# Kernel tuning notes

Measured on AMD Instinct MI355X. Metric: run time of the kernel, lower is better.

The kernel has to match this reference:

```python
import jax, jax.numpy as jnp
import numpy as np

B_SZ = 2
D_MODEL = 1024
H = 16
C = 8
BLK = 128
DK = 64
DV = 64
NCHUNK = 1024            # tokens per chunk (divisible by BLK)
T = C * (1 + NCHUNK)     # 8200: [g0, chunk0..., g1, chunk1..., ...]


def setup_inputs() -> dict:
    key = jax.random.key(0)
    k0, k1, k2, k3, k4 = jax.random.split(key, 5)
    s = 0.02
    x  = jax.random.normal(k0, (B_SZ, T, D_MODEL), dtype=jnp.float32)
    Wq = jax.random.normal(k1, (D_MODEL, H * DK), dtype=jnp.float32) * s
    Wk = jax.random.normal(k2, (D_MODEL, H * DK), dtype=jnp.float32) * s
    Wv = jax.random.normal(k3, (D_MODEL, H * DV), dtype=jnp.float32) * s
    Wo = jax.random.normal(k4, (H * DV, D_MODEL), dtype=jnp.float32) * s
    bo = jnp.zeros((D_MODEL,), dtype=jnp.float32)
    return {"x": x, "Wq": Wq, "Wk": Wk, "Wv": Wv, "Wo": Wo, "bo": bo}


def _local_sparse_3block(qf, kf, vf):
    # qf,kf: [BC, H, N, dk], vf: [BC, H, N, dv]; window = [left, current, right] blocks
    bc, h, n, dk = qf.shape
    dv = vf.shape[-1]
    nb = n // BLK
    q = qf.reshape(bc, h, nb, BLK, dk)
    k = kf.reshape(bc, h, nb, BLK, dk)
    v = vf.reshape(bc, h, nb, BLK, dv)
    zk = jnp.zeros((bc, h, 1, BLK, dk), qf.dtype)
    zv = jnp.zeros((bc, h, 1, BLK, dv), qf.dtype)
    kp = jnp.concatenate([zk, k, zk], axis=2)          # [bc,h,nb+2,B,dk]
    vp = jnp.concatenate([zv, v, zv], axis=2)
    k_win = jnp.concatenate([kp[:, :, 0:nb], kp[:, :, 1:nb + 1], kp[:, :, 2:nb + 2]], axis=3)  # [bc,h,nb,3B,dk]
    v_win = jnp.concatenate([vp[:, :, 0:nb], vp[:, :, 1:nb + 1], vp[:, :, 2:nb + 2]], axis=3)  # [bc,h,nb,3B,dv]
    scale = 1.0 / np.sqrt(dk).astype(np.float32)
    scores = jnp.einsum('bhnqd,bhnkd->bhnqk', q, k_win) * scale   # [bc,h,nb,B,3B]
    mask = np.zeros((nb, 3 * BLK), dtype=bool)
    mask[0, :BLK] = True           # first block: left padding invalid
    mask[-1, 2 * BLK:] = True      # last block: right padding invalid
    scores = jnp.where(jnp.asarray(mask)[None, None, :, None, :], -jnp.inf, scores)
    attn = jax.nn.softmax(scores, axis=-1)
    out = jnp.einsum('bhnqk,bhnkd->bhnqd', attn, v_win)
    return out.reshape(bc, h, n, dv)


def reference(x, Wq, Wk, Wv, Wo, bo):
    Bb, Tt, _ = x.shape
    q = (x @ Wq).reshape(Bb, Tt, H, DK).transpose(0, 2, 1, 3)  # [B,H,T,dk]
    k = (x @ Wk).reshape(Bb, Tt, H, DK).transpose(0, 2, 1, 3)
    v = (x @ Wv).reshape(Bb, Tt, H, DV).transpose(0, 2, 1, 3)
    stride = NCHUNK + 1
    g_idx = jnp.arange(C) * stride
    gq = q[:, :, g_idx]  # [B,H,C,dk]
    gk = k[:, :, g_idx]
    gv = v[:, :, g_idx]  # [B,H,C,dv]
    local_idx = ((g_idx + 1)[:, None] + jnp.arange(NCHUNK)[None, :]).reshape(-1)
    qx = q[:, :, local_idx].reshape(Bb, H, C, NCHUNK, DK)
    kx = k[:, :, local_idx].reshape(Bb, H, C, NCHUNK, DK)
    vx = v[:, :, local_idx].reshape(Bb, H, C, NCHUNK, DV)
    # local 3-block attention per chunk
    q_flat = qx.transpose(0, 2, 1, 3, 4).reshape(Bb * C, H, NCHUNK, DK)
    k_flat = kx.transpose(0, 2, 1, 3, 4).reshape(Bb * C, H, NCHUNK, DK)
    v_flat = vx.transpose(0, 2, 1, 3, 4).reshape(Bb * C, H, NCHUNK, DV)
    out_local = _local_sparse_3block(q_flat, k_flat, v_flat)
    out_local = out_local.reshape(Bb, C, H, NCHUNK, DV).transpose(0, 2, 1, 3, 4)  # [B,H,C,Nchunk,dv]
    # each local token additionally receives its chunk's global value directly
    out_chunks = out_local + gv[:, :, :, None, :]
    # global tokens attend over all globals + own chunk's locals (joint softmax, fp32)
    scale = 1.0 / np.sqrt(DK).astype(np.float32)
    scores_gg = jnp.einsum('bhcd,bhed->bhce', gq, gk) * scale      # [B,H,C,C]
    scores_gl = jnp.einsum('bhcd,bhcnd->bhcn', gq, kx) * scale     # [B,H,C,Nchunk]
    attn = jax.nn.softmax(jnp.concatenate([scores_gg, scores_gl], axis=-1), axis=-1)
    a_gg, a_gl = attn[..., :C], attn[..., C:]
    out_g = (jnp.einsum('bhce,bhed->bhcd', a_gg, gv)
             + jnp.einsum('bhcn,bhcnd->bhcd', a_gl, vx))           # [B,H,C,dv]
    out_inter = jnp.concatenate([out_g[:, :, :, None, :], out_chunks], axis=3)  # [B,H,C,1+Nchunk,dv]
    out = out_inter.reshape(Bb, H, Tt, DV).transpose(0, 2, 1, 3).reshape(Bb, Tt, H * DV)
    return out @ Wo + bo
```

## Files before the change

kernel.cpp:

```cpp
#include <hip/hip_runtime.h>
#include <hip/hip_bf16.h>

typedef __bf16 bf16x8 __attribute__((ext_vector_type(8)));
typedef float  f32x4  __attribute__((ext_vector_type(4)));
typedef unsigned short u16x8 __attribute__((ext_vector_type(8)));
typedef unsigned short u16x4 __attribute__((ext_vector_type(4)));
typedef unsigned u32x4 __attribute__((ext_vector_type(4)));
typedef unsigned long long u64x2 __attribute__((ext_vector_type(2)));

#define T_TOK   8200
#define M_TOK   16400
#define QKV_LD  3072
#define DM      1024

#define AS1CU const __attribute__((address_space(1))) unsigned int*
#define AS3U  __attribute__((address_space(3))) unsigned int*
#define GLDS16(g, s) __builtin_amdgcn_global_load_lds((AS1CU)(g), (AS3U)(s), 16, 0, 0)

__device__ __forceinline__ unsigned short f2bf(float f){
  __hip_bfloat16 h = __float2bfloat16(f);
  return *reinterpret_cast<unsigned short*>(&h);
}
__device__ __forceinline__ float bf2f(unsigned short u){
  union { unsigned u; float f; } x; x.u = ((unsigned)u) << 16;
  return x.f;
}

__global__ __launch_bounds__(256) void k_prep(const float* __restrict__ x, unsigned short* __restrict__ xb,
                                              const float* __restrict__ Wq, const float* __restrict__ Wk,
                                              const float* __restrict__ Wv, const float* __restrict__ Wo,
                                              unsigned short* __restrict__ wqkvt, unsigned short* __restrict__ wot){
  __shared__ float t[64][65];
  int bid = blockIdx.x, tid = threadIdx.x;
  if (bid < 2048){
    const long n4 = (long)M_TOK * 1024 / 4;
    long i = (long)bid * 256 + tid;
    const long stride = 2048L * 256;
    for (long e = i; e < n4; e += stride){
      float4 v = ((const float4*)x)[e];
      u16x4 o; o[0]=f2bf(v.x); o[1]=f2bf(v.y); o[2]=f2bf(v.z); o[3]=f2bf(v.w);
      ((u16x4*)xb)[e] = o;
    }
    return;
  }
  int bid2 = bid - 2048;
  int z = bid2 & 3; int rest = bid2 >> 2;
  int bx = rest & 15, by = rest >> 4;
  const float* W; unsigned short* Wt;
  if      (z == 0){ W = Wq; Wt = wqkvt; }
  else if (z == 1){ W = Wk; Wt = wqkvt + (size_t)1024*1024; }
  else if (z == 2){ W = Wv; Wt = wqkvt + (size_t)2048*1024; }
  else            { W = Wo; Wt = wot; }
  int tk0 = bx * 64, tn0 = by * 64;
#pragma unroll
  for (int i = 0; i < 4; i++){
    int ch = tid + i*256; int kr = ch >> 4, n4i = (ch & 15) * 4;
    float4 v = *(const float4*)(W + (size_t)(tk0+kr)*1024 + tn0 + n4i);
    t[kr][n4i+0]=v.x; t[kr][n4i+1]=v.y; t[kr][n4i+2]=v.z; t[kr][n4i+3]=v.w;
  }
  __syncthreads();
#pragma unroll
  for (int i = 0; i < 4; i++){
    int ch = tid + i*256; int nr = ch >> 4, k4 = (ch & 15) * 4;
    u16x4 o;
#pragma unroll
    for (int e = 0; e < 4; e++) o[e] = f2bf(t[k4+e][nr]);
    *(u16x4*)(Wt + (size_t)(tn0+nr)*1024 + tk0 + k4) = o;
  }
}

__global__ __launch_bounds__(256,2) void k_gemm(const unsigned short* __restrict__ A,
                                                const unsigned short* __restrict__ Bt,
                                                const float* __restrict__ bias,
                                                void* __restrict__ Cout,
                                                int M, int K, int ldc, int bf16out, int gn){
  __shared__ unsigned short As[128][64];
  __shared__ unsigned short Bs[128][64];
  int tid = threadIdx.x, l = tid & 63, w = tid >> 6;
  int li = l & 15, lh = l >> 4;
  int nwg = gridDim.x;
  int wg = (blockIdx.x & 7) * (nwg >> 3) + (blockIdx.x >> 3);
  int m0 = (wg / gn) * 128, n0 = (wg % gn) * 128;
  int wm = (w & 1) * 64, wn = (w >> 1) * 64;
  int lr = l >> 3, lc = l & 7;
  int lsw = li & 7;

  f32x4 acc[4][4];
#pragma unroll
  for (int a = 0; a < 4; a++)
#pragma unroll
    for (int b = 0; b < 4; b++) acc[a][b] = 0.f;

  for (int kt = 0; kt < K; kt += 64){
    __syncthreads();
#pragma unroll
    for (int i = 0; i < 4; i++){
      int r = w*32 + i*8 + lr;
      int colsw = (lc ^ (r & 7)) * 8;
      int rga = m0 + r; if (rga >= M) rga = M - 1;
      GLDS16(A  + (size_t)rga     *K + kt + colsw, &As[w*32 + i*8][0]);
      GLDS16(Bt + (size_t)(n0 + r)*K + kt + colsw, &Bs[w*32 + i*8][0]);
    }
    __syncthreads();
#pragma unroll
    for (int ks = 0; ks < 2; ks++){
      bf16x8 af[4], bfr[4];
#pragma unroll
      for (int mt = 0; mt < 4; mt++)
        af[mt] = *(const bf16x8*)&As[wm + mt*16 + li][((ks*4 + lh) ^ lsw) * 8];
#pragma unroll
      for (int nt = 0; nt < 4; nt++)
        bfr[nt] = *(const bf16x8*)&Bs[wn + nt*16 + li][((ks*4 + lh) ^ lsw) * 8];
#pragma unroll
      for (int mt = 0; mt < 4; mt++)
#pragma unroll
        for (int nt = 0; nt < 4; nt++)
          acc[mt][nt] = __builtin_amdgcn_mfma_f32_16x16x32_bf16(af[mt], bfr[nt], acc[mt][nt], 0, 0, 0);
    }
  }
#pragma unroll
  for (int mt = 0; mt < 4; mt++)
#pragma unroll
    for (int nt = 0; nt < 4; nt++)
#pragma unroll
      for (int r = 0; r < 4; r++){
        int row = m0 + wm + mt*16 + lh*4 + r;
        int col = n0 + wn + nt*16 + li;
        if (row < M){
          float v = acc[mt][nt][r] + (bias ? bias[col] : 0.f);
          if (bf16out) ((unsigned short*)Cout)[(size_t)row*ldc + col] = f2bf(v);
          else         ((float*)Cout)[(size_t)row*ldc + col] = v;
        }
      }
}

__global__ __launch_bounds__(256,3) void k_local(const unsigned short* __restrict__ qkv,
                                                 unsigned short* __restrict__ att){
  __shared__ unsigned short Ks[128][64];
  __shared__ unsigned short Vt[64][136];

  int tid = threadIdx.x;

  if (blockIdx.x < 256){
    float* sc   = (float*)&Ks[0][0];
    float* red  = sc + 1032;
    float* gq_s = red + 256;
    int gid = blockIdx.x;
    int c = gid & 7, h = (gid >> 3) & 15, b = gid >> 7;
    size_t bT = (size_t)b * T_TOK;
    size_t grow = bT + (size_t)c*1025;
    if (tid < 64) gq_s[tid] = bf2f(qkv[grow*QKV_LD + h*64 + tid]);
    __syncthreads();
    float lmax = -3e38f;
    for (int idx = tid; idx < 1032; idx += 256){
      size_t krow = (idx < 8) ? (bT + (size_t)idx*1025) : (bT + (size_t)c*1025 + 1 + (idx - 8));
      const unsigned short* kp = qkv + krow*QKV_LD + 1024 + h*64;
      float s = 0.f;
#pragma unroll
      for (int d0 = 0; d0 < 64; d0 += 8){
        u16x8 kv = *(const u16x8*)(kp + d0);
#pragma unroll
        for (int e = 0; e < 8; e++) s += gq_s[d0+e] * bf2f(kv[e]);
      }
      s *= 0.125f;
      sc[idx] = s;
      lmax = fmaxf(lmax, s);
    }
    red[tid] = lmax; __syncthreads();
    for (int st = 128; st > 0; st >>= 1){ if (tid < st) red[tid] = fmaxf(red[tid], red[tid+st]); __syncthreads(); }
    float m = red[0]; __syncthreads();
    float lsum = 0.f;
    for (int idx = tid; idx < 1032; idx += 256){
      float p = __expf(sc[idx] - m); sc[idx] = p; lsum += p;
    }
    red[tid] = lsum; __syncthreads();
    for (int st = 128; st > 0; st >>= 1){ if (tid < st) red[tid] += red[tid+st]; __syncthreads(); }
    float denom = red[0]; __syncthreads();
    int d = tid & 63, part = tid >> 6;
    float acc = 0.f;
    for (int idx = part; idx < 1032; idx += 4){
      size_t krow = (idx < 8) ? (bT + (size_t)idx*1025) : (bT + (size_t)c*1025 + 1 + (idx - 8));
      acc += sc[idx] * bf2f(qkv[krow*QKV_LD + 2048 + h*64 + d]);
    }
    red[tid] = acc; __syncthreads();
    if (tid < 64){
      float o = (red[tid] + red[tid+64] + red[tid+128] + red[tid+192]) / denom;
      att[grow*DM + h*64 + tid] = f2bf(o);
    }
    return;
  }

  int l = tid & 63, w = tid >> 6;
  int li = l & 15, lh = l >> 4;
  int lr = l >> 3, lc = l & 7;
  int lsw = li & 7;
  int wg0 = blockIdx.x - 256;
  int wg = (wg0 & 7) * 256 + (wg0 >> 3);
  int blk = wg & 7, c = (wg >> 3) & 7, h = (wg >> 6) & 15, b = wg >> 10;
  size_t bT = (size_t)b * T_TOK;
  int tokq0 = c*1025 + 1 + blk*128;

  bf16x8 aq[2][2];
#pragma unroll
  for (int tr = 0; tr < 2; tr++)
#pragma unroll
    for (int ks = 0; ks < 2; ks++)
      aq[tr][ks] = *(const bf16x8*)(qkv + (bT + tokq0 + w*32 + tr*16 + li)*QKV_LD + h*64 + ks*32 + lh*8);

  float psum[2] = {0.f, 0.f};
  f32x4 oacc[2][4];
#pragma unroll
  for (int tr = 0; tr < 2; tr++)
#pragma unroll
    for (int ct = 0; ct < 4; ct++) oacc[tr][ct] = 0.f;

  for (int kb = blk-1; kb <= blk+1; ++kb){
    if ((unsigned)kb > 7u) continue;
    int tokk0 = c*1025 + 1 + kb*128;

    u16x8 vlo[2], vhi[2];
#pragma unroll
    for (int i = 0; i < 2; i++){
      int gv = 4*i + w;
      const unsigned short* vp = qkv + (bT + tokk0 + 2*l)*QKV_LD + 2048 + h*64 + gv*8;
      vlo[i] = *(const u16x8*)vp;
      vhi[i] = *(const u16x8*)(vp + QKV_LD);
    }
    __syncthreads();
#pragma unroll
    for (int i = 0; i < 4; i++){
      int r = w*32 + i*8 + lr;
      int colk = (lc ^ (r & 7)) * 8;
      GLDS16(qkv + (bT + tokk0 + r)*QKV_LD + 1024 + h*64 + colk, &Ks[w*32 + i*8][0]);
    }
#pragma unroll
    for (int i = 0; i < 2; i++)
#pragma unroll
      for (int e = 0; e < 8; e++){
        unsigned pk = (unsigned)vlo[i][e] | ((unsigned)vhi[i][e] << 16);
        *(unsigned*)&Vt[(4*i + w)*8 + e][2*l] = pk;
      }
    __syncthreads();

    f32x4 s2[2][8];
#pragma unroll
    for (int tr = 0; tr < 2; tr++)
#pragma unroll
      for (int ct = 0; ct < 8; ct++) s2[tr][ct] = 0.f;
#pragma unroll
    for (int ct = 0; ct < 8; ct++)
#pragma unroll
      for (int ks = 0; ks < 2; ks++){
        bf16x8 kf = *(const bf16x8*)&Ks[ct*16 + li][((ks*4 + lh) ^ lsw) * 8];
        s2[0][ct] = __builtin_amdgcn_mfma_f32_16x16x32_bf16(kf, aq[0][ks], s2[0][ct], 0, 0, 0);
        s2[1][ct] = __builtin_amdgcn_mfma_f32_16x16x32_bf16(kf, aq[1][ks], s2[1][ct], 0, 0, 0);
      }

#pragma unroll
    for (int ks = 0; ks < 4; ks++){
      bf16x8 pa[2];
#pragma unroll
      for (int tr = 0; tr < 2; tr++){
        float q0 = __expf(s2[tr][2*ks  ][0] * 0.125f);
        float q1 = __expf(s2[tr][2*ks  ][1] * 0.125f);
        float q2 = __expf(s2[tr][2*ks  ][2] * 0.125f);
        float q3 = __expf(s2[tr][2*ks  ][3] * 0.125f);
        float q4 = __expf(s2[tr][2*ks+1][0] * 0.125f);
        float q5 = __expf(s2[tr][2*ks+1][1] * 0.125f);
        float q6 = __expf(s2[tr][2*ks+1][2] * 0.125f);
        float q7 = __expf(s2[tr][2*ks+1][3] * 0.125f);
        psum[tr] += ((q0 + q1) + (q2 + q3)) + ((q4 + q5) + (q6 + q7));
        u32x4 frv;
        frv.x = (unsigned)f2bf(q0) | ((unsigned)f2bf(q1) << 16);
        frv.y = (unsigned)f2bf(q2) | ((unsigned)f2bf(q3) << 16);
        frv.z = (unsigned)f2bf(q4) | ((unsigned)f2bf(q5) << 16);
        frv.w = (unsigned)f2bf(q6) | ((unsigned)f2bf(q7) << 16);
        pa[tr] = __builtin_bit_cast(bf16x8, frv);
      }
      int base = ks*16 + 2*lh;
#pragma unroll
      for (int ct = 0; ct < 4; ct++){
        const unsigned* vrow = (const unsigned*)&Vt[ct*16 + li][0];
        u64x2 vfv;
        vfv.x = *(const unsigned long long*)(vrow + base);
        vfv.y = *(const unsigned long long*)(vrow + base + 8);
        bf16x8 vf = __builtin_bit_cast(bf16x8, vfv);
        oacc[0][ct] = __builtin_amdgcn_mfma_f32_16x16x32_bf16(pa[0], vf, oacc[0][ct], 0, 0, 0);
        oacc[1][ct] = __builtin_amdgcn_mfma_f32_16x16x32_bf16(pa[1], vf, oacc[1][ct], 0, 0, 0);
      }
    }
  }

#pragma unroll
  for (int tr = 0; tr < 2; tr++){
    psum[tr] += __shfl_xor(psum[tr], 16, 64);
    psum[tr] += __shfl_xor(psum[tr], 32, 64);
  }
  float ps[2][4];
#pragma unroll
  for (int tr = 0; tr < 2; tr++)
#pragma unroll
    for (int r = 0; r < 4; r++)
      ps[tr][r] = __shfl(psum[tr], lh*4 + r, 64);
  float gvv[4];
#pragma unroll
  for (int ct = 0; ct < 4; ct++)
    gvv[ct] = bf2f(qkv[(bT + c*1025)*QKV_LD + 2048 + h*64 + ct*16 + li]);
#pragma unroll
  for (int tr = 0; tr < 2; tr++)
#pragma unroll
    for (int ct = 0; ct < 4; ct++)
#pragma unroll
      for (int r = 0; r < 4; r++){
        int row = w*32 + tr*16 + lh*4 + r;
        float v = oacc[tr][ct][r] / ps[tr][r] + gvv[ct];
        att[(bT + tokq0 + row)*DM + h*64 + ct*16 + li] = f2bf(v);
      }
}

extern "C" void kernel_launch(void* const* d_in, const int* in_sizes, int n_in,
                              void* d_out, int out_size, void* d_ws, size_t ws_size,
                              hipStream_t stream) {
  const float* x  = (const float*)d_in[0];
  const float* Wq = (const float*)d_in[1];
  const float* Wk = (const float*)d_in[2];
  const float* Wv = (const float*)d_in[3];
  const float* Wo = (const float*)d_in[4];
  const float* bo = (const float*)d_in[5];
  float* out = (float*)d_out;

  unsigned short* xb    = (unsigned short*)d_ws;
  unsigned short* wqkvt = xb    + (size_t)M_TOK * 1024;
  unsigned short* wot   = wqkvt + (size_t)3072 * 1024;
  unsigned short* qkv   = wot   + (size_t)1024 * 1024;
  unsigned short* att   = qkv   + (size_t)M_TOK * QKV_LD;

  k_prep<<<3072, 256, 0, stream>>>(x, xb, Wq, Wk, Wv, Wo, wqkvt, wot);
  k_gemm<<<dim3(129*24), 256, 0, stream>>>(xb, wqkvt, (const float*)nullptr, (void*)qkv,
                                           M_TOK, 1024, QKV_LD, 1, 24);
  k_local<<<2304, 256, 0, stream>>>(qkv, att);
  k_gemm<<<dim3(129*8), 256, 0, stream>>>(att, wot, bo, (void*)out,
                                          M_TOK, 1024, DM, 0, 8);
}
```

Measured before the change: 296.9 us.

## Double-buffer GEMM LDS tiles and raise wave priority around MFMA blocks

The GEMM kernel now keeps two LDS buffers for the A and B tiles. It issues the global-to-LDS loads for the next K tile before computing on the current one, so memory latency overlaps with the MFMA work, and it needs only one barrier per iteration instead of two. It also wraps the MFMA block in s_setprio to favour the compute waves. The cost is double the LDS use (64KB per block), which may limit occupancy under launch_bounds(256,2). Correctness relies on the compiler inserting vmcnt waits before the barrier.

```diff
diff --git a/kernel.cpp b/kernel.cpp
--- a/kernel.cpp
+++ b/kernel.cpp
@@ -74,8 +74,8 @@
                                                 const float* __restrict__ bias,
                                                 void* __restrict__ Cout,
                                                 int M, int K, int ldc, int bf16out, int gn){
-  __shared__ unsigned short As[128][64];
-  __shared__ unsigned short Bs[128][64];
+  __shared__ unsigned short As[2][128][64];
+  __shared__ unsigned short Bs[2][128][64];
   int tid = threadIdx.x, l = tid & 63, w = tid >> 6;
   int li = l & 15, lh = l >> 4;
   int nwg = gridDim.x;
@@ -85,49 +85,61 @@
   int lr = l >> 3, lc = l & 7;
   int lsw = li & 7;
 
+#define STAGE(buf, kt) do{ \
+    _Pragma("unroll") \
+    for (int i_ = 0; i_ < 4; i_++){ \
+      int r_ = w*32 + i_*8 + lr; \
+      int colsw_ = (lc ^ (r_ & 7)) * 8; \
+      int rga_ = m0 + r_; if (rga_ >= M) rga_ = M - 1; \
+      GLDS16(A  + (size_t)rga_     *K + (kt) + colsw_, &As[buf][w*32 + i_*8][0]); \
+      GLDS16(Bt + (size_t)(n0 + r_)*K + (kt) + colsw_, &Bs[buf][w*32 + i_*8][0]); \
+    } }while(0)
+
   f32x4 acc[4][4];
 #pragma unroll
   for (int a = 0; a < 4; a++)
 #pragma unroll
     for (int b = 0; b < 4; b++) acc[a][b] = 0.f;
 
-  for (int kt = 0; kt < K; kt += 64){
-    __syncthreads();
-#pragma unroll
-    for (int i = 0; i < 4; i++){
-      int r = w*32 + i*8 + lr;
-      int colsw = (lc ^ (r & 7)) * 8;
-      int rga = m0 + r; if (rga >= M) rga = M - 1;
-      GLDS16(A  + (size_t)rga     *K + kt + colsw, &As[w*32 + i*8][0]);
-      GLDS16(Bt + (size_t)(n0 + r)*K + kt + colsw, &Bs[w*32 + i*8][0]);
-    }
-    __syncthreads();
+  STAGE(0, 0);
+  __syncthreads();
+
+  int nt = K >> 6;
+  int cur = 0;
+  for (int t = 0; t < nt; ++t){
+    if (t + 1 < nt) STAGE(cur ^ 1, (t + 1) * 64);
 #pragma unroll
     for (int ks = 0; ks < 2; ks++){
       bf16x8 af[4], bfr[4];
 #pragma unroll
       for (int mt = 0; mt < 4; mt++)
-        af[mt] = *(const bf16x8*)&As[wm + mt*16 + li][((ks*4 + lh) ^ lsw) * 8];
-#pragma unroll
-      for (int nt = 0; nt < 4; nt++)
-        bfr[nt] = *(const bf16x8*)&Bs[wn + nt*16 + li][((ks*4 + lh) ^ lsw) * 8];
+        af[mt] = *(const bf16x8*)&As[cur][wm + mt*16 + li][((ks*4 + lh) ^ lsw) * 8];
+#pragma unroll
+      for (int nt2 = 0; nt2 < 4; nt2++)
+        bfr[nt2] = *(const bf16x8*)&Bs[cur][wn + nt2*16 + li][((ks*4 + lh) ^ lsw) * 8];
+      __builtin_amdgcn_s_setprio(1);
 #pragma unroll
       for (int mt = 0; mt < 4; mt++)
 #pragma unroll
-        for (int nt = 0; nt < 4; nt++)
-          acc[mt][nt] = __builtin_amdgcn_mfma_f32_16x16x32_bf16(af[mt], bfr[nt], acc[mt][nt], 0, 0, 0);
-    }
-  }
+        for (int nt2 = 0; nt2 < 4; nt2++)
+          acc[mt][nt2] = __builtin_amdgcn_mfma_f32_16x16x32_bf16(af[mt], bfr[nt2], acc[mt][nt2], 0, 0, 0);
+      __builtin_amdgcn_s_setprio(0);
+    }
+    __syncthreads();
+    cur ^= 1;
+  }
+#undef STAGE
+
 #pragma unroll
   for (int mt = 0; mt < 4; mt++)
 #pragma unroll
-    for (int nt = 0; nt < 4; nt++)
+    for (int nt2 = 0; nt2 < 4; nt2++)
 #pragma unroll
       for (int r = 0; r < 4; r++){
         int row = m0 + wm + mt*16 + lh*4 + r;
-        int col = n0 + wn + nt*16 + li;
+        int col = n0 + wn + nt2*16 + li;
         if (row < M){
-          float v = acc[mt][nt][r] + (bias ? bias[col] : 0.f);
+          float v = acc[mt][nt2][r] + (bias ? bias[col] : 0.f);
           if (bf16out) ((unsigned short*)Cout)[(size_t)row*ldc + col] = f2bf(v);
           else         ((float*)Cout)[(size_t)row*ldc + col] = v;
         }
```

Measured after the change: 355.7 us. 1.2x slower.
